# Kernel tuning notes

Measured on AMD Instinct MI355X. Metric: run time of the kernel, lower is better.

Reference implementation:

```python
import jax, jax.numpy as jnp
import numpy as np

N = 16384      # total nodes in batched graph
B = 64         # number of graphs (dgl.batch)
DEG = 8        # random in-degree (self-loops added on top)
C = 128        # feature width
H = 2          # heads in middle blocks
EH = 8         # E: heads of attn_seq / codebook entries
DEPTH = 2
IN = 8         # max_node_color (one-hot input width)
NE = N * DEG + N  # edges incl. self-loops


def layernorm(x, g, b, eps=1e-5):
    mu = jnp.mean(x, axis=-1, keepdims=True)
    var = jnp.mean(jnp.square(x - mu), axis=-1, keepdims=True)
    return (x - mu) * jax.lax.rsqrt(var + eps) * g + b


def gatv2(x, src, dst, Ws, bs, Wd, bd, attn):
    # DGL GATv2Conv (eval mode, attn_drop inactive, share_weights=False)
    h, c = attn.shape
    n = x.shape[0]
    el = (x @ Ws + bs).reshape(n, h, c)   # fc_src
    er = (x @ Wd + bd).reshape(n, h, c)   # fc_dst
    e = jax.nn.leaky_relu(el[src] + er[dst], negative_slope=0.2)  # [E,h,c]
    logits = jnp.einsum('ehc,hc->eh', e, attn)                    # [E,h]
    # edge softmax over incoming edges of each dst node
    m = jax.ops.segment_max(logits, dst, num_segments=n)
    a = jnp.exp(logits - m[dst])
    z = jax.ops.segment_sum(a, dst, num_segments=n)
    a = a / z[dst]
    return jax.ops.segment_sum(el[src] * a[..., None], dst, num_segments=n)  # [n,h,c]


def setup_inputs() -> dict:
    key = jax.random.key(0)
    ks = iter(jax.random.split(key, 64))
    nrm = lambda *s: jax.random.normal(next(ks), s, jnp.float32) * 0.05
    colors = jax.random.randint(next(ks), (N,), 0, IN)
    feats = jax.nn.one_hot(colors, IN, dtype=jnp.float32)
    loops = jnp.arange(N)
    src = jnp.concatenate([jax.random.randint(next(ks), (N * DEG,), 0, N), loops])
    dst = jnp.concatenate([jax.random.randint(next(ks), (N * DEG,), 0, N), loops])
    graph_ids = jnp.arange(N) // (N // B)
    inp = dict(feats=feats, src=src, dst=dst, graph_ids=graph_ids)
    # attn_up: GATv2Conv(IN -> C, 1 head)
    inp.update(up_Ws=nrm(IN, C), up_bs=nrm(C), up_Wd=nrm(IN, C), up_bd=nrm(C), up_attn=nrm(1, C))
    # depth blocks: GATv2Conv(C -> C, H heads) + ff
    inp.update(L_Ws=nrm(DEPTH, C, H * C), L_bs=nrm(DEPTH, H * C),
               L_Wd=nrm(DEPTH, C, H * C), L_bd=nrm(DEPTH, H * C),
               L_attn=nrm(DEPTH, H, C),
               ff_ln_g=jnp.ones((DEPTH, C), jnp.float32), ff_ln_b=jnp.zeros((DEPTH, C), jnp.float32),
               ff_W1=nrm(DEPTH, C, 2 * C), ff_b1=nrm(DEPTH, 2 * C),
               ff_W2=nrm(DEPTH, 2 * C, C), ff_b2=nrm(DEPTH, C),
               ff_W3=nrm(DEPTH, H * C, C), ff_b3=nrm(DEPTH, C))
    # attn_seq: GATv2Conv(C -> C, EH heads) + ff_seq
    inp.update(seq_Ws=nrm(C, EH * C), seq_bs=nrm(EH * C),
               seq_Wd=nrm(C, EH * C), seq_bd=nrm(EH * C),
               seq_attn=nrm(EH, C),
               fs_ln_g=jnp.ones((C,), jnp.float32), fs_ln_b=jnp.zeros((C,), jnp.float32),
               fs_W1=nrm(C, 2 * C), fs_b1=nrm(2 * C),
               fs_W2=nrm(2 * C, C), fs_b2=nrm(C),
               gate_W=nrm(EH * C, 1), gate_b=nrm(1))
    return inp


def reference(feats, src, dst, graph_ids,
              up_Ws, up_bs, up_Wd, up_bd, up_attn,
              L_Ws, L_bs, L_Wd, L_bd, L_attn,
              ff_ln_g, ff_ln_b, ff_W1, ff_b1, ff_W2, ff_b2, ff_W3, ff_b3,
              seq_Ws, seq_bs, seq_Wd, seq_bd, seq_attn,
              fs_ln_g, fs_ln_b, fs_W1, fs_b1, fs_W2, fs_b2,
              gate_W, gate_b):
    # attn_up (1 head) -> flatten to [N, C]
    x = gatv2(feats, src, dst, up_Ws, up_bs, up_Wd, up_bd, up_attn).reshape(N, C)
    for l in range(DEPTH):
        h = gatv2(x, src, dst, L_Ws[l], L_bs[l], L_Wd[l], L_bd[l], L_attn[l])  # [N,H,C]
        h = layernorm(h, ff_ln_g[l], ff_ln_b[l])
        h = jax.nn.gelu(h @ ff_W1[l] + ff_b1[l], approximate=False)
        h = h @ ff_W2[l] + ff_b2[l]                              # [N,H,C]
        x = h.reshape(N, H * C) @ ff_W3[l] + ff_b3[l]            # [N,C]
    y = gatv2(x, src, dst, seq_Ws, seq_bs, seq_Wd, seq_bd, seq_attn)  # [N,EH,C]
    y = layernorm(y, fs_ln_g, fs_ln_b)
    y = jax.nn.gelu(y @ fs_W1 + fs_b1, approximate=False) @ fs_W2 + fs_b2
    y = y.reshape(N, EH * C)
    # GlobalAttentionPooling: softmax(gate) over nodes within each graph
    gate = y @ gate_W + gate_b                                   # [N,1]
    gm = jax.ops.segment_max(gate, graph_ids, num_segments=B)
    ga = jnp.exp(gate - gm[graph_ids])
    gz = jax.ops.segment_sum(ga, graph_ids, num_segments=B)
    ga = ga / gz[graph_ids]
    pooled = jax.ops.segment_sum(ga * y, graph_ids, num_segments=B)  # [B, EH*C]
    return jnp.tanh(pooled.reshape(B, EH, C))
```

## Files before the change

kernel.cpp:

```cpp
#include <hip/hip_runtime.h>
#include <hip/hip_bf16.h>

typedef __hip_bfloat16 bf16;
typedef __attribute__((ext_vector_type(8))) short short8;
typedef __attribute__((ext_vector_type(4))) float f32x4;

#define NN 16384
#define NB 64
#define NE_TOT (NN*8 + NN)
#define CW 128

__device__ __forceinline__ float b2f(bf16 x){ return __bfloat162float(x); }
__device__ __forceinline__ bf16  f2b(float x){ return __float2bfloat16(x); }
__device__ __forceinline__ float lrelu(float x){ return fmaxf(x, 0.2f*x); }
__device__ __forceinline__ float gelu_f(float x){ return 0.5f*x*(1.f + erff(x*0.70710678118654752f)); }
__device__ __forceinline__ float us2f(unsigned int u){ return __uint_as_float(u << 16); }
__device__ __forceinline__ unsigned short f2us(float x){ return __builtin_bit_cast(unsigned short, f2b(x)); }

__device__ __forceinline__ void async16(const void* g, void* l){
  __builtin_amdgcn_global_load_lds((const __attribute__((address_space(1))) void*)g,
                                   (__attribute__((address_space(3))) void*)l, 16, 0, 0);
}

__global__ void k_detect(const unsigned short* __restrict__ f, int* __restrict__ flag){
  __shared__ int cnt;
  if(threadIdx.x == 0) cnt = 0;
  __syncthreads();
  int c = 0;
  for(int i = threadIdx.x; i < 2048; i += 256)
    if(f[2*i] == 0x3F80) c++;
  atomicAdd(&cnt, c);
  __syncthreads();
  if(threadIdx.x == 0) *flag = (cnt > 0) ? 0 : 1;
}

struct ConvArgs { const void* in[32]; bf16* out[32]; int n[32]; int tk[32]; int tj[32]; int ls[32]; };
__global__ __launch_bounds__(256) void k_conv_all(ConvArgs a, const int* __restrict__ flag){
  int which = blockIdx.y;
  int t = blockIdx.x*256 + threadIdx.x;
  int n = a.n[which];
  if(t >= n) return;
  float v = (*flag) ? ((const float*)a.in[which])[t] : b2f(((const bf16*)a.in[which])[t]);
  int tj = a.tj[which];
  if(tj == 0){ a.out[which][t] = f2b(v); return; }
  int tk = a.tk[which], kj = tk*tj;
  int l = t / kj, r = t - l*kj;
  int k = r / tj, j = r - k*tj;
  a.out[which][l*a.ls[which] + j*tk + k] = f2b(v);
}

__global__ void k_zero2(int* __restrict__ a, int* __restrict__ b, int n){
  int i = blockIdx.x*blockDim.x + threadIdx.x;
  if(i < n){ a[i] = 0; b[i] = 0; }
}
__global__ void k_hist(const int* __restrict__ dst, int* __restrict__ deg, int ne){
  int e = blockIdx.x*blockDim.x + threadIdx.x;
  if(e < ne) atomicAdd(&deg[dst[e]], 1);
}
__global__ void k_scan(const int* __restrict__ deg, int* __restrict__ off){
  __shared__ int s[256];
  int t = threadIdx.x;
  const int chunk = NN/256;
  int base = t*chunk;
  int sum = 0;
  for(int i=0;i<chunk;i++) sum += deg[base+i];
  s[t] = sum; __syncthreads();
  for(int o=1;o<256;o<<=1){
    int v = (t >= o) ? s[t-o] : 0;
    __syncthreads();
    s[t] += v;
    __syncthreads();
  }
  int run = (t == 0) ? 0 : s[t-1];
  for(int i=0;i<chunk;i++){ off[base+i] = run; run += deg[base+i]; }
  if(t == 255) off[NN] = run;
}
__global__ void k_scatter(const int* __restrict__ src, const int* __restrict__ dst,
                          const int* __restrict__ off, int* __restrict__ cursor,
                          int* __restrict__ csr_src, int ne){
  int e = blockIdx.x*blockDim.x + threadIdx.x;
  if(e < ne){
    int d = dst[e];
    int p = off[d] + atomicAdd(&cursor[d], 1);
    csr_src[p] = src[e];
  }
}

__global__ __launch_bounds__(128) void k_up(const bf16* __restrict__ feats,
    const bf16* __restrict__ Ws, const bf16* __restrict__ bs,
    const bf16* __restrict__ Wd, const bf16* __restrict__ bd,
    bf16* __restrict__ eler){
  int n = blockIdx.x, c = threadIdx.x;
  __shared__ float f[8];
  if(c < 8) f[c] = b2f(feats[n*8 + c]);
  __syncthreads();
  float a = b2f(bs[c]), b = b2f(bd[c]);
  #pragma unroll
  for(int k=0;k<8;k++){
    float fv = f[k];
    a += fv*b2f(Ws[k*CW + c]);
    b += fv*b2f(Wd[k*CW + c]);
  }
  eler[(size_t)n*256 + c]       = f2b(a);
  eler[(size_t)n*256 + 128 + c] = f2b(b);
}

template<int ACT>
__global__ __launch_bounds__(256) void k_mm(
    const bf16* __restrict__ A, int gshA, int gstrA,
    const bf16* __restrict__ WT, const bf16* __restrict__ bias,
    bf16* __restrict__ C, int gshC, int gstrC,
    int K, int J){
  __shared__ char smem[32768];
  short* As = (short*)smem;
  short* Bs = (short*)(smem + 16384);
  int tid = threadIdx.x, w = tid >> 6, lane = tid & 63;
  int l15 = lane & 15, q = lane >> 4;
  int wm = w >> 1, wn = w & 1;
  int bm = blockIdx.y*128, bn = blockIdx.x*128;

  f32x4 acc[4][4];
  #pragma unroll
  for(int i=0;i<4;i++)
    #pragma unroll
    for(int j=0;j<4;j++) acc[i][j] = (f32x4)0.f;

  int srow = w*32 + (lane >> 2);
  int scol = (lane & 3)*8;
  const bf16* gA[2]; const bf16* gB[2];
  short* lA[2]; short* lB[2];
  int mskA = (1 << gshA) - 1;
  #pragma unroll
  for(int a=0;a<2;a++){
    int rowA = bm + srow + a*16;
    gA[a] = A  + (size_t)(rowA >> gshA)*(size_t)gstrA + (size_t)(rowA & mskA)*K + scol;
    gB[a] = WT + (size_t)(bn + srow + a*16)*K + scol;
    lA[a] = As + (w*32 + a*16)*32;
    lB[a] = Bs + (w*32 + a*16)*32;
  }

  for(int kt=0; kt<K; kt+=64){
    #pragma unroll
    for(int a=0;a<2;a++)
      #pragma unroll
      for(int kh=0;kh<2;kh++){
        async16(gA[a] + kt + kh*32, lA[a] + kh*4096);
        async16(gB[a] + kt + kh*32, lB[a] + kh*4096);
      }
    __syncthreads();
    #pragma unroll
    for(int kh=0;kh<2;kh++){
      short8 af[4], bfr[4];
      #pragma unroll
      for(int i=0;i<4;i++) af[i]  = *(short8*)&As[kh*4096 + (wm*64 + i*16 + l15)*32 + q*8];
      #pragma unroll
      for(int j=0;j<4;j++) bfr[j] = *(short8*)&Bs[kh*4096 + (wn*64 + j*16 + l15)*32 + q*8];
      #pragma unroll
      for(int i=0;i<4;i++)
        #pragma unroll
        for(int j=0;j<4;j++)
          acc[i][j] = __builtin_amdgcn_mfma_f32_16x16x32_bf16(af[i], bfr[j], acc[i][j], 0, 0, 0);
    }
    __syncthreads();
  }

  float* ep = (float*)(smem + w*4352);
  int rr = lane >> 2;
  int cc = (lane & 3)*16;
  int mskC = (1 << gshC) - 1;
  #pragma unroll
  for(int i=0;i<4;i++){
    #pragma unroll
    for(int j=0;j<4;j++){
      float bv = b2f(bias[bn + wn*64 + j*16 + l15]);
      #pragma unroll
      for(int r=0;r<4;r++){
        float v = acc[i][j][r] + bv;
        if(ACT == 1) v = gelu_f(v);
        ep[(q*4+r)*68 + j*16 + l15] = v;
      }
    }
    float4 v0 = *(float4*)&ep[rr*68 + cc];
    float4 v1 = *(float4*)&ep[rr*68 + cc + 4];
    float4 v2 = *(float4*)&ep[rr*68 + cc + 8];
    float4 v3 = *(float4*)&ep[rr*68 + cc + 12];
    float vv[16] = {v0.x,v0.y,v0.z,v0.w, v1.x,v1.y,v1.z,v1.w,
                    v2.x,v2.y,v2.z,v2.w, v3.x,v3.y,v3.z,v3.w};
    unsigned int u[8];
    #pragma unroll
    for(int k=0;k<8;k++)
      u[k] = (unsigned int)f2us(vv[2*k]) | ((unsigned int)f2us(vv[2*k+1]) << 16);
    int row = bm + wm*64 + i*16 + rr;
    bf16* cp = C + (size_t)(row >> gshC)*(size_t)gstrC + (size_t)(row & mskC)*J + bn + wn*64 + cc;
    *(uint4*)cp       = make_uint4(u[0],u[1],u[2],u[3]);
    *(uint4*)(cp + 8) = make_uint4(u[4],u[5],u[6],u[7]);
  }
}

template<int E>
__device__ __forceinline__ void load_row(const bf16* p, float* f){
  if constexpr (E == 2){
    unsigned int v = *(const unsigned int*)p;
    f[0] = us2f(v & 0xffffu); f[1] = __uint_as_float(v & 0xffff0000u);
  } else if constexpr (E == 4){
    uint2 v = *(const uint2*)p;
    f[0] = us2f(v.x & 0xffffu); f[1] = __uint_as_float(v.x & 0xffff0000u);
    f[2] = us2f(v.y & 0xffffu); f[3] = __uint_as_float(v.y & 0xffff0000u);
  } else {
    uint4 a = *(const uint4*)p;
    uint4 b = *(const uint4*)(p + 8);
    unsigned int vs[8] = {a.x,a.y,a.z,a.w,b.x,b.y,b.z,b.w};
    #pragma unroll
    for(int i=0;i<8;i++){
      f[2*i]   = us2f(vs[i] & 0xffffu);
      f[2*i+1] = __uint_as_float(vs[i] & 0xffff0000u);
    }
  }
}
template<int E>
__device__ __forceinline__ void store_row(bf16* p, const float* f){
  unsigned int vs[E/2];
  #pragma unroll
  for(int i=0;i<E/2;i++)
    vs[i] = (unsigned int)f2us(f[2*i]) | ((unsigned int)f2us(f[2*i+1]) << 16);
  if constexpr (E == 2){ *(unsigned int*)p = vs[0]; }
  else if constexpr (E == 4){ *(uint2*)p = make_uint2(vs[0], vs[1]); }
  else {
    *(uint4*)p       = make_uint4(vs[0], vs[1], vs[2], vs[3]);
    *(uint4*)(p + 8) = make_uint4(vs[4], vs[5], vs[6], vs[7]);
  }
}

template<int H, bool LNF>
__global__ __launch_bounds__(256) void k_gat(const int* __restrict__ off, const int* __restrict__ csr_src,
    const bf16* __restrict__ el, const bf16* __restrict__ er, const bf16* __restrict__ attn,
    const bf16* __restrict__ lng, const bf16* __restrict__ lnb, bf16* __restrict__ out,
    int rs_in, int rs_out){
  constexpr int EPL = 2*H;
  constexpr int G   = 64/H;
  int w = threadIdx.x >> 6, lane = threadIdx.x & 63;
  int n = blockIdx.x*4 + w;

  float ef[EPL], af[EPL];
  load_row<EPL>(er   + (size_t)n*rs_in + lane*EPL, ef);
  load_row<EPL>(attn + lane*EPL, af);

  int p0 = off[n], p1 = off[n+1];

  float m = -1e30f, z = 0.f;
  float acc[EPL];
  #pragma unroll
  for(int e=0;e<EPL;e++) acc[e] = 0.f;

  float xf[EPL];
  int s0 = csr_src[p0];
  load_row<EPL>(el + (size_t)s0*rs_in + lane*EPL, xf);
  for(int p = p0; p < p1; p++){
    float xn[EPL];
    if(p + 1 < p1){
      int sn = csr_src[p+1];
      load_row<EPL>(el + (size_t)sn*rs_in + lane*EPL, xn);
    }
    float part = 0.f;
    #pragma unroll
    for(int e=0;e<EPL;e++) part += af[e]*lrelu(xf[e] + ef[e]);
    #pragma unroll
    for(int o=G/2; o; o>>=1) part += __shfl_xor(part, o, 64);
    float nm = fmaxf(m, part);
    float alpha = expf(m - nm);
    float c = expf(part - nm);
    z = z*alpha + c;
    #pragma unroll
    for(int e=0;e<EPL;e++) acc[e] = acc[e]*alpha + c*xf[e];
    m = nm;
    #pragma unroll
    for(int e=0;e<EPL;e++) xf[e] = xn[e];
  }
  float rz = 1.f/z;
  #pragma unroll
  for(int e=0;e<EPL;e++) acc[e] *= rz;

  if constexpr (LNF){
    float sl = 0.f;
    #pragma unroll
    for(int e=0;e<EPL;e++) sl += acc[e];
    #pragma unroll
    for(int o=G/2; o; o>>=1) sl += __shfl_xor(sl, o, 64);
    float mu = sl*(1.f/128.f);
    float qs = 0.f;
    #pragma unroll
    for(int e=0;e<EPL;e++){ float d = acc[e] - mu; qs += d*d; }
    #pragma unroll
    for(int o=G/2; o; o>>=1) qs += __shfl_xor(qs, o, 64);
    float r = rsqrtf(qs*(1.f/128.f) + 1e-5f);
    int cbase = (lane & (G-1))*EPL;
    #pragma unroll
    for(int e=0;e<EPL;e++)
      acc[e] = (acc[e] - mu)*r*b2f(lng[cbase + e]) + b2f(lnb[cbase + e]);
  }
  store_row<EPL>(out + (size_t)n*rs_out + lane*EPL, acc);
}

__global__ __launch_bounds__(256) void k_gate(const bf16* __restrict__ y2, const bf16* __restrict__ gW,
                                              const bf16* __restrict__ gb, float* __restrict__ gate){
  int n = blockIdx.x*4 + (threadIdx.x >> 6);
  int lane = threadIdx.x & 63;
  const bf16* yr = y2 + (size_t)n*2048;
  float p = 0.f;
  #pragma unroll
  for(int j=0;j<16;j++) p += b2f(yr[lane + j*64])*b2f(gW[lane + j*64]);
  #pragma unroll
  for(int o=32;o;o>>=1) p += __shfl_down(p, o, 64);
  if(lane == 0) gate[n] = p + b2f(gb[0]);
}

__global__ __launch_bounds__(64) void k_pool1(const float* __restrict__ gate,
                                              float* __restrict__ gm, float* __restrict__ gz){
  int g = blockIdx.x, lane = threadIdx.x;
  float v0 = gate[g*256 + lane], v1 = gate[g*256 + 64 + lane];
  float v2 = gate[g*256 + 128 + lane], v3 = gate[g*256 + 192 + lane];
  float m = fmaxf(fmaxf(v0,v1), fmaxf(v2,v3));
  #pragma unroll
  for(int o=32;o;o>>=1) m = fmaxf(m, __shfl_xor(m, o, 64));
  float z = expf(v0-m) + expf(v1-m) + expf(v2-m) + expf(v3-m);
  #pragma unroll
  for(int o=32;o;o>>=1) z += __shfl_xor(z, o, 64);
  if(lane == 0){ gm[g] = m; gz[g] = z; }
}

__global__ __launch_bounds__(256) void k_pool2(const float* __restrict__ gate,
    const float* __restrict__ gm, const float* __restrict__ gz,
    const bf16* __restrict__ y2, void* __restrict__ outv, const int* __restrict__ flag){
  int g = blockIdx.x >> 2, cb = blockIdx.x & 3, t = threadIdx.x;
  __shared__ float aL[256];
  aL[t] = expf(gate[g*256 + t] - gm[g]) / gz[g];
  __syncthreads();
  int ch = cb*256 + t;
  float acc = 0.f;
  const bf16* base = y2 + (size_t)g*256*2048 + ch;
  for(int i=0;i<256;i++) acc += aL[i]*b2f(base[(size_t)i*2048]);
  float v = tanhf(acc);
  size_t idx = (size_t)g*1024 + ch;
  if(*flag) ((float*)outv)[idx] = v;
  else      ((bf16*)outv)[idx] = f2b(v);
}

extern "C" void kernel_launch(void* const* d_in, const int* in_sizes, int n_in,
                              void* d_out, int out_size, void* d_ws, size_t ws_size,
                              hipStream_t stream){
  const int* src = (const int*)d_in[1];
  const int* dst = (const int*)d_in[2];

  char* wsb = (char*)d_ws;
  size_t o = 0;
  auto take = [&](size_t bytes)->char*{
    char* p = wsb + o; o = (o + bytes + 255) & ~(size_t)255; return p;
  };
  int*   flag  = (int*)take(4);
  float* gate  = (float*)take((size_t)NN*4);
  float* gm    = (float*)take(64*4);
  float* gz    = (float*)take(64*4);
  int* deg     = (int*)take((size_t)NN*4);
  int* cursor  = (int*)take((size_t)NN*4);
  int* off     = (int*)take((size_t)(NN+1)*4);
  int* csr_src = (int*)take((size_t)NE_TOT*4);

  bf16* WcombL   = (bf16*)take((size_t)2*512*128*2);
  bf16* bcombL   = (bf16*)take((size_t)2*512*2);
  bf16* WcombSeq = (bf16*)take((size_t)2048*128*2);
  bf16* bcombSeq = (bf16*)take((size_t)2048*2);

  ConvArgs ca;
  const int fidx[32] = {0, 4,5,6,7,8, 9,10,11,12,13, 14,15,16,17,18,19,20,21,
                        22,23,24,25,26, 27,28,29,30,31,32, 33,34};
  bf16* cp[32];
  int maxn = 0;
  for(int i=0;i<32;i++){
    int n = in_sizes[fidx[i]];
    ca.in[i] = d_in[fidx[i]]; ca.n[i] = n;
    ca.tk[i] = 0; ca.tj[i] = 0; ca.ls[i] = 0;
    cp[i] = nullptr;
    if(n > maxn) maxn = n;
  }
  auto plain = [&](int i){ cp[i] = (bf16*)take((size_t)ca.n[i]*2); ca.out[i] = cp[i]; };
  auto spec  = [&](int i, bf16* dst_, int tk, int tj, int ls){
    ca.out[i] = dst_; ca.tk[i] = tk; ca.tj[i] = tj; ca.ls[i] = ls; cp[i] = dst_; };
  auto owntr = [&](int i, int tk, int tj){
    cp[i] = (bf16*)take((size_t)ca.n[i]*2);
    ca.out[i] = cp[i]; ca.tk[i] = tk; ca.tj[i] = tj; ca.ls[i] = tk*tj; };

  plain(0);
  plain(1); plain(2); plain(3); plain(4); plain(5);
  spec(6,  WcombL,          128, 256, 65536);
  spec(7,  bcombL,          256, 1,   512);
  spec(8,  WcombL + 32768,  128, 256, 65536);
  spec(9,  bcombL + 256,    256, 1,   512);
  plain(10); plain(11); plain(12);
  owntr(13, 128, 256);
  plain(14);
  owntr(15, 256, 128); plain(16);
  owntr(17, 256, 128); plain(18);
  spec(19, WcombSeq,           128, 1024, 131072);
  spec(20, bcombSeq,           1024, 1,  2048);
  spec(21, WcombSeq + 131072,  128, 1024, 131072);
  spec(22, bcombSeq + 1024,    1024, 1,  2048);
  plain(23); plain(24); plain(25);
  owntr(26, 128, 256); plain(27);
  owntr(28, 256, 128); plain(29);
  plain(30); plain(31);

  bf16* AB = (bf16*)take((size_t)NN*2048*2);
  bf16* X  = (bf16*)take((size_t)NN*128*2);
  size_t bigT = (size_t)131072*256*2, smallT = (size_t)32768*256*2;
  bool useBigT = (ws_size - o) >= bigT + 4096;
  bf16* T = (bf16*)take(useBigT ? bigT : smallT);

  bf16* G1 = AB + (size_t)NN*1024;
  bf16* G2 = AB + (size_t)NN*1024 + (size_t)NN*256;

  k_detect<<<1, 256, 0, stream>>>((const unsigned short*)d_in[0], flag);
  k_conv_all<<<dim3((maxn+255)/256, 32), 256, 0, stream>>>(ca, flag);

  k_zero2 <<<(NN+255)/256, 256, 0, stream>>>(deg, cursor, NN);
  k_hist  <<<(NE_TOT+255)/256, 256, 0, stream>>>(dst, deg, NE_TOT);
  k_scan  <<<1, 256, 0, stream>>>(deg, off);
  k_scatter<<<(NE_TOT+255)/256, 256, 0, stream>>>(src, dst, off, cursor, csr_src, NE_TOT);

  k_up<<<NN, 128, 0, stream>>>(cp[0], cp[1], cp[2], cp[3], cp[4], AB);
  k_gat<1,false><<<NN/4, 256, 0, stream>>>(off, csr_src, AB, AB + 128, cp[5],
                                           nullptr, nullptr, X, 256, 128);

  for(int l=0; l<2; l++){
    k_mm<0><<<dim3(4, 128), 256, 0, stream>>>(X, 30, 0, WcombL + l*65536, bcombL + l*512,
                                              AB, 30, 0, 128, 512);
    k_gat<2,true><<<NN/4, 256, 0, stream>>>(off, csr_src, AB, AB + 256, cp[10] + l*256,
                                            cp[11] + l*128, cp[12] + l*128, G1, 512, 256);
    k_mm<1><<<dim3(2, 256), 256, 0, stream>>>(G1, 30, 0, cp[13] + l*32768, cp[14] + l*256,
                                              T, 30, 0, 128, 256);
    k_mm<0><<<dim3(1, 256), 256, 0, stream>>>(T, 30, 0, cp[15] + l*32768, cp[16] + l*128,
                                              G2, 30, 0, 256, 128);
    k_mm<0><<<dim3(1, 128), 256, 0, stream>>>(G2, 30, 0, cp[17] + l*32768, cp[18] + l*128,
                                              X, 30, 0, 256, 128);
  }

  k_mm<0><<<dim3(16, 128), 256, 0, stream>>>(X, 30, 0, WcombSeq, bcombSeq, AB, 30, 0, 128, 2048);
  k_gat<8,true><<<NN/4, 256, 0, stream>>>(off, csr_src, AB, AB + 1024, cp[23],
                                          cp[24], cp[25], AB + 1024, 2048, 2048);
  if(useBigT){
    k_mm<1><<<dim3(2, 1024), 256, 0, stream>>>(AB + 1024, 3, 2048, cp[26], cp[27], T, 30, 0, 128, 256);
    k_mm<0><<<dim3(1, 1024), 256, 0, stream>>>(T, 30, 0, cp[28], cp[29], AB, 3, 2048, 256, 128);
  } else {
    for(int c=0; c<4; c++){
      bf16* base = AB + (size_t)c*4096*2048;
      k_mm<1><<<dim3(2, 256), 256, 0, stream>>>(base + 1024, 3, 2048, cp[26], cp[27], T, 30, 0, 128, 256);
      k_mm<0><<<dim3(1, 256), 256, 0, stream>>>(T, 30, 0, cp[28], cp[29], base, 3, 2048, 256, 128);
    }
  }

  k_gate <<<NN/4, 256, 0, stream>>>(AB, cp[30], cp[31], gate);
  k_pool1<<<NB, 64, 0, stream>>>(gate, gm, gz);
  k_pool2<<<NB*4, 256, 0, stream>>>(gate, gm, gz, AB, d_out, flag);
  (void)n_in; (void)out_size;
}
```

Measured before the change: 514.5 us.

## Fuse feed-forward GEMM pair into one kernel and split GAT heads across waves

Adds a k_ff kernel that computes the 128->256 GELU layer and the 256->128 projection for 32 rows per block, keeping the hidden activations in LDS. This removes the global temporary T and one kernel launch per block. k_gat gains a head-split template parameter, so each wave handles half the heads of a node and the grid doubles. That raises parallelism and lowers per-lane registers, at the cost of re-reading CSR indices and gathering twice per node.

```diff
diff --git a/kernel.cpp b/kernel.cpp
--- a/kernel.cpp
+++ b/kernel.cpp
@@ -197,6 +197,107 @@
   }
 }
 
+__global__ __launch_bounds__(256) void k_ff(
+    const bf16* __restrict__ A, int gshA, int gstrA,
+    const bf16* __restrict__ W1T, const bf16* __restrict__ b1,
+    const bf16* __restrict__ W2T, const bf16* __restrict__ b2,
+    bf16* __restrict__ C, int gshC, int gstrC){
+  __shared__ short Wb[8704];
+  __shared__ short Hs[8320];
+  int tid = threadIdx.x, w = tid >> 6, lane = tid & 63;
+  int l15 = lane & 15, q = lane >> 4;
+  int bm = blockIdx.x*32;
+  int mskA = (1 << gshA) - 1, mskC = (1 << gshC) - 1;
+  int mt = w & 1, jg = w >> 1;
+
+  int rowA = bm + mt*16 + l15;
+  const bf16* ap = A + (size_t)(rowA >> gshA)*(size_t)gstrA + (size_t)(rowA & mskA)*128;
+  short8 af[4];
+  #pragma unroll
+  for(int ki=0;ki<4;ki++) af[ki] = *(const short8*)&ap[ki*32 + q*8];
+
+  for(int jt=0; jt<4; jt++){
+    #pragma unroll
+    for(int it=0;it<4;it++){
+      int slot = tid + it*256;
+      int r = slot >> 4, c8 = slot & 15;
+      *(int4*)&Wb[r*132 + c8*8] = *(const int4*)&W1T[(size_t)(jt*64 + r)*128 + c8*8];
+    }
+    __syncthreads();
+    f32x4 acc1[2] = {(f32x4)0.f, (f32x4)0.f};
+    #pragma unroll
+    for(int ki=0;ki<4;ki++){
+      #pragma unroll
+      for(int t=0;t<2;t++){
+        int jrow = (jg*2 + t)*16 + l15;
+        short8 bfr = *(short8*)&Wb[jrow*132 + ki*32 + q*8];
+        acc1[t] = __builtin_amdgcn_mfma_f32_16x16x32_bf16(af[ki], bfr, acc1[t], 0, 0, 0);
+      }
+    }
+    #pragma unroll
+    for(int t=0;t<2;t++){
+      int jcol = jt*64 + (jg*2 + t)*16 + l15;
+      float bv = b2f(b1[jcol]);
+      #pragma unroll
+      for(int r=0;r<4;r++){
+        float v = gelu_f(acc1[t][r] + bv);
+        Hs[(mt*16 + q*4 + r)*260 + jcol] = (short)f2us(v);
+      }
+    }
+    __syncthreads();
+  }
+
+  f32x4 acc2[4];
+  #pragma unroll
+  for(int t=0;t<4;t++) acc2[t] = (f32x4)0.f;
+  for(int kc=0; kc<4; kc++){
+    #pragma unroll
+    for(int it=0;it<4;it++){
+      int slot = tid + it*256;
+      int r = slot >> 3, c8 = slot & 7;
+      *(int4*)&Wb[r*68 + c8*8] = *(const int4*)&W2T[(size_t)r*256 + kc*64 + c8*8];
+    }
+    __syncthreads();
+    #pragma unroll
+    for(int ki=0;ki<2;ki++){
+      short8 haf = *(short8*)&Hs[(mt*16 + l15)*260 + kc*64 + ki*32 + q*8];
+      #pragma unroll
+      for(int t=0;t<4;t++){
+        int jrow = (jg*4 + t)*16 + l15;
+        short8 bfr = *(short8*)&Wb[jrow*68 + ki*32 + q*8];
+        acc2[t] = __builtin_amdgcn_mfma_f32_16x16x32_bf16(haf, bfr, acc2[t], 0, 0, 0);
+      }
+    }
+    __syncthreads();
+  }
+
+  float* epf = (float*)Hs;
+  #pragma unroll
+  for(int t=0;t<4;t++){
+    int jcol = (jg*4 + t)*16 + l15;
+    float bv = b2f(b2[jcol]);
+    #pragma unroll
+    for(int r=0;r<4;r++)
+      epf[(mt*16 + q*4 + r)*130 + jcol] = acc2[t][r] + bv;
+  }
+  __syncthreads();
+  int row = tid >> 3, cseg = (tid & 7)*16;
+  float4 v0 = *(float4*)&epf[row*130 + cseg];
+  float4 v1 = *(float4*)&epf[row*130 + cseg + 4];
+  float4 v2 = *(float4*)&epf[row*130 + cseg + 8];
+  float4 v3 = *(float4*)&epf[row*130 + cseg + 12];
+  float vv[16] = {v0.x,v0.y,v0.z,v0.w, v1.x,v1.y,v1.z,v1.w,
+                  v2.x,v2.y,v2.z,v2.w, v3.x,v3.y,v3.z,v3.w};
+  unsigned int u[8];
+  #pragma unroll
+  for(int k=0;k<8;k++)
+    u[k] = (unsigned int)f2us(vv[2*k]) | ((unsigned int)f2us(vv[2*k+1]) << 16);
+  int rowC = bm + row;
+  bf16* cpb = C + (size_t)(rowC >> gshC)*(size_t)gstrC + (size_t)(rowC & mskC)*128 + cseg;
+  *(uint4*)cpb       = make_uint4(u[0],u[1],u[2],u[3]);
+  *(uint4*)(cpb + 8) = make_uint4(u[4],u[5],u[6],u[7]);
+}
+
 template<int E>
 __device__ __forceinline__ void load_row(const bf16* p, float* f){
   if constexpr (E == 2){
@@ -206,6 +307,14 @@
     uint2 v = *(const uint2*)p;
     f[0] = us2f(v.x & 0xffffu); f[1] = __uint_as_float(v.x & 0xffff0000u);
     f[2] = us2f(v.y & 0xffffu); f[3] = __uint_as_float(v.y & 0xffff0000u);
+  } else if constexpr (E == 8){
+    uint4 a = *(const uint4*)p;
+    unsigned int vs[4] = {a.x,a.y,a.z,a.w};
+    #pragma unroll
+    for(int i=0;i<4;i++){
+      f[2*i]   = us2f(vs[i] & 0xffffu);
+      f[2*i+1] = __uint_as_float(vs[i] & 0xffff0000u);
+    }
   } else {
     uint4 a = *(const uint4*)p;
     uint4 b = *(const uint4*)(p + 8);
@@ -225,27 +334,30 @@
     vs[i] = (unsigned int)f2us(f[2*i]) | ((unsigned int)f2us(f[2*i+1]) << 16);
   if constexpr (E == 2){ *(unsigned int*)p = vs[0]; }
   else if constexpr (E == 4){ *(uint2*)p = make_uint2(vs[0], vs[1]); }
+  else if constexpr (E == 8){ *(uint4*)p = make_uint4(vs[0], vs[1], vs[2], vs[3]); }
   else {
     *(uint4*)p       = make_uint4(vs[0], vs[1], vs[2], vs[3]);
     *(uint4*)(p + 8) = make_uint4(vs[4], vs[5], vs[6], vs[7]);
   }
 }
 
-template<int H, bool LNF>
+template<int H, bool LNF, int SSH>
 __global__ __launch_bounds__(256) void k_gat(const int* __restrict__ off, const int* __restrict__ csr_src,
     const bf16* __restrict__ el, const bf16* __restrict__ er, const bf16* __restrict__ attn,
     const bf16* __restrict__ lng, const bf16* __restrict__ lnb, bf16* __restrict__ out,
-    int rs_in, int rs_out){
+    int rsn_in, int rsh_in, int rsn_out, int rsh_out){
   constexpr int EPL = 2*H;
   constexpr int G   = 64/H;
   int w = threadIdx.x >> 6, lane = threadIdx.x & 63;
-  int n = blockIdx.x*4 + w;
+  int nv = blockIdx.x*4 + w;
+  int node = nv >> SSH, hf = nv & ((1 << SSH) - 1);
+  size_t hin = (size_t)hf*rsh_in;
 
   float ef[EPL], af[EPL];
-  load_row<EPL>(er   + (size_t)n*rs_in + lane*EPL, ef);
-  load_row<EPL>(attn + lane*EPL, af);
-
-  int p0 = off[n], p1 = off[n+1];
+  load_row<EPL>(er + (size_t)node*rsn_in + hin + lane*EPL, ef);
+  load_row<EPL>(attn + hf*(64*EPL) + lane*EPL, af);
+
+  int p0 = off[node], p1 = off[node+1];
 
   float m = -1e30f, z = 0.f;
   float acc[EPL];
@@ -254,12 +366,12 @@
 
   float xf[EPL];
   int s0 = csr_src[p0];
-  load_row<EPL>(el + (size_t)s0*rs_in + lane*EPL, xf);
+  load_row<EPL>(el + (size_t)s0*rsn_in + hin + lane*EPL, xf);
   for(int p = p0; p < p1; p++){
     float xn[EPL];
     if(p + 1 < p1){
       int sn = csr_src[p+1];
-      load_row<EPL>(el + (size_t)sn*rs_in + lane*EPL, xn);
+      load_row<EPL>(el + (size_t)sn*rsn_in + hin + lane*EPL, xn);
     }
     float part = 0.f;
     #pragma unroll
@@ -298,7 +410,7 @@
     for(int e=0;e<EPL;e++)
       acc[e] = (acc[e] - mu)*r*b2f(lng[cbase + e]) + b2f(lnb[cbase + e]);
   }
-  store_row<EPL>(out + (size_t)n*rs_out + lane*EPL, acc);
+  store_row<EPL>(out + (size_t)node*rsn_out + (size_t)hf*rsh_out + lane*EPL, acc);
 }
 
 __global__ __launch_bounds__(256) void k_gate(const bf16* __restrict__ y2, const bf16* __restrict__ gW,
@@ -411,12 +523,9 @@
 
   bf16* AB = (bf16*)take((size_t)NN*2048*2);
   bf16* X  = (bf16*)take((size_t)NN*128*2);
-  size_t bigT = (size_t)131072*256*2, smallT = (size_t)32768*256*2;
-  bool useBigT = (ws_size - o) >= bigT + 4096;
-  bf16* T = (bf16*)take(useBigT ? bigT : smallT);
-
   bf16* G1 = AB + (size_t)NN*1024;
   bf16* G2 = AB + (size_t)NN*1024 + (size_t)NN*256;
+  (void)ws_size; (void)n_in; (void)out_size;
 
   k_detect<<<1, 256, 0, stream>>>((const unsigned short*)d_in[0], flag);
   k_conv_all<<<dim3((maxn+255)/256, 32), 256, 0, stream>>>(ca, flag);
@@ -427,38 +536,29 @@
   k_scatter<<<(NE_TOT+255)/256, 256, 0, stream>>>(src, dst, off, cursor, csr_src, NE_TOT);
 
   k_up<<<NN, 128, 0, stream>>>(cp[0], cp[1], cp[2], cp[3], cp[4], AB);
-  k_gat<1,false><<<NN/4, 256, 0, stream>>>(off, csr_src, AB, AB + 128, cp[5],
-                                           nullptr, nullptr, X, 256, 128);
+  k_gat<1,false,0><<<NN/4, 256, 0, stream>>>(off, csr_src, AB, AB + 128, cp[5],
+                                             nullptr, nullptr, X, 256, 0, 128, 0);
 
   for(int l=0; l<2; l++){
     k_mm<0><<<dim3(4, 128), 256, 0, stream>>>(X, 30, 0, WcombL + l*65536, bcombL + l*512,
                                               AB, 30, 0, 128, 512);
-    k_gat<2,true><<<NN/4, 256, 0, stream>>>(off, csr_src, AB, AB + 256, cp[10] + l*256,
-                                            cp[11] + l*128, cp[12] + l*128, G1, 512, 256);
-    k_mm<1><<<dim3(2, 256), 256, 0, stream>>>(G1, 30, 0, cp[13] + l*32768, cp[14] + l*256,
-                                              T, 30, 0, 128, 256);
-    k_mm<0><<<dim3(1, 256), 256, 0, stream>>>(T, 30, 0, cp[15] + l*32768, cp[16] + l*128,
-                                              G2, 30, 0, 256, 128);
+    k_gat<1,true,1><<<2*NN/4, 256, 0, stream>>>(off, csr_src, AB, AB + 256, cp[10] + l*256,
+                                                cp[11] + l*128, cp[12] + l*128, G1,
+                                                512, 128, 256, 128);
+    k_ff<<<2*NN/32, 256, 0, stream>>>(G1, 30, 0, cp[13] + l*32768, cp[14] + l*256,
+                                      cp[15] + l*32768, cp[16] + l*128, G2, 30, 0);
     k_mm<0><<<dim3(1, 128), 256, 0, stream>>>(G2, 30, 0, cp[17] + l*32768, cp[18] + l*128,
                                               X, 30, 0, 256, 128);
   }
 
   k_mm<0><<<dim3(16, 128), 256, 0, stream>>>(X, 30, 0, WcombSeq, bcombSeq, AB, 30, 0, 128, 2048);
-  k_gat<8,true><<<NN/4, 256, 0, stream>>>(off, csr_src, AB, AB + 1024, cp[23],
-                                          cp[24], cp[25], AB + 1024, 2048, 2048);
-  if(useBigT){
-    k_mm<1><<<dim3(2, 1024), 256, 0, stream>>>(AB + 1024, 3, 2048, cp[26], cp[27], T, 30, 0, 128, 256);
-    k_mm<0><<<dim3(1, 1024), 256, 0, stream>>>(T, 30, 0, cp[28], cp[29], AB, 3, 2048, 256, 128);
-  } else {
-    for(int c=0; c<4; c++){
-      bf16* base = AB + (size_t)c*4096*2048;
-      k_mm<1><<<dim3(2, 256), 256, 0, stream>>>(base + 1024, 3, 2048, cp[26], cp[27], T, 30, 0, 128, 256);
-      k_mm<0><<<dim3(1, 256), 256, 0, stream>>>(T, 30, 0, cp[28], cp[29], base, 3, 2048, 256, 128);
-    }
-  }
+  k_gat<4,true,1><<<2*NN/4, 256, 0, stream>>>(off, csr_src, AB, AB + 1024, cp[23],
+                                              cp[24], cp[25], AB + 1024,
+                                              2048, 512, 2048, 512);
+  k_ff<<<131072/32, 256, 0, stream>>>(AB + 1024, 3, 2048, cp[26], cp[27],
+                                      cp[28], cp[29], AB, 3, 2048);
 
   k_gate <<<NN/4, 256, 0, stream>>>(AB, cp[30], cp[31], gate);
   k_pool1<<<NB, 64, 0, stream>>>(gate, gm, gz);
   k_pool2<<<NB*4, 256, 0, stream>>>(gate, gm, gz, AB, d_out, flag);
-  (void)n_in; (void)out_size;
-}
+}
```

After: 546.2 us. +6.2%, slower.
